# Optimization experiments

Measured on AMD Instinct MI355X. Metric: run time of the kernel, lower is better.

The kernel has to match this reference:

```python
import math
import jax, jax.numpy as jnp
import numpy as np

NUM_HEADS = 8
NUM_LANDMARKS = 64
MP_ITERS = 6


def moore_penrose_iter_pinv(x, iters=MP_ITERS):
    # x: [..., m, m]; iterative Newton-Schulz-style pseudo-inverse
    abs_x = jnp.abs(x)
    col = abs_x.sum(axis=-1)
    row = abs_x.sum(axis=-2)
    z = jnp.swapaxes(x, -1, -2) / (jnp.max(col) * jnp.max(row))
    I = jnp.eye(x.shape[-1], dtype=x.dtype)
    for _ in range(iters):
        xz = x @ z
        z = 0.25 * z @ (13.0 * I - xz @ (15.0 * I - xz @ (7.0 * I - xz)))
    return z


def setup_inputs() -> dict:
    key = jax.random.key(0)
    k_x, k_qkv, k_proj = jax.random.split(key, 3)
    B, T, E = 2, 2048, 512
    x = jax.random.normal(k_x, (B, T, E), dtype=jnp.float32)
    w_qkv = jax.random.normal(k_qkv, (E, 3 * E), dtype=jnp.float32) * 0.02
    b_qkv = jnp.zeros((3 * E,), dtype=jnp.float32)
    w_proj = jax.random.normal(k_proj, (E, E), dtype=jnp.float32) * 0.02
    b_proj = jnp.zeros((E,), dtype=jnp.float32)
    return {"x": x, "w_qkv": w_qkv, "b_qkv": b_qkv, "w_proj": w_proj, "b_proj": b_proj}


def reference(x, w_qkv, b_qkv, w_proj, b_proj):
    B, T, E = x.shape
    H = NUM_HEADS
    M = NUM_LANDMARKS
    hd = E // H
    # T chosen as a multiple of M so the original pad branch is a no-op
    qkv = x @ w_qkv + b_qkv  # [B,T,3E]
    q, k, v = jnp.split(qkv, 3, axis=-1)

    def to_heads(t):
        return t.reshape(B, T, H, hd).transpose(0, 2, 1, 3)  # [B,H,T,hd]

    q = to_heads(q) * (1.0 / math.sqrt(hd))
    k = to_heads(k)
    v = to_heads(v)

    l = T // M  # landmark group size
    q_landmarks = q.reshape(B, H, M, l, hd).mean(axis=3)  # [B,H,M,hd]
    k_landmarks = k.reshape(B, H, M, l, hd).mean(axis=3)  # [B,H,M,hd]

    q_kl = jnp.einsum('bhid,bhjd->bhij', q, k_landmarks)           # [B,H,T,M]
    ql_kl = jnp.einsum('bhid,bhjd->bhij', q_landmarks, k_landmarks)  # [B,H,M,M]
    ql_k = jnp.einsum('bhid,bhjd->bhij', q_landmarks, k)           # [B,H,M,T]

    neg_inf = float('-inf')
    mask_q_kl = jnp.tril(jnp.ones((T, M), dtype=bool))
    mask_ql_kl = jnp.tril(jnp.ones((M, M), dtype=bool))
    mask_ql_k = jnp.tril(jnp.ones((M, T), dtype=bool))

    F_t = jax.nn.softmax(jnp.where(mask_q_kl, q_kl, neg_inf), axis=-1)    # [B,H,T,M]
    A = jax.nn.softmax(jnp.where(mask_ql_kl, ql_kl, neg_inf), axis=-1)    # [B,H,M,M]
    B_t = jax.nn.softmax(jnp.where(mask_ql_k, ql_k, neg_inf), axis=-1)    # [B,H,M,T]

    A_t = moore_penrose_iter_pinv(A, iters=MP_ITERS)

    attn = (F_t @ A_t) @ B_t  # [B,H,T,T] (original materializes this for dropout)
    y = attn @ v              # [B,H,T,hd]
    y = y.transpose(0, 2, 1, 3).reshape(B, T, E)
    return y @ w_proj + b_proj
```

## Files before the change

kernel.cpp:

```cpp
#include <hip/hip_runtime.h>
#include <hip/hip_bf16.h>

#define TB 2048
#define EB 512

using short8 = __attribute__((ext_vector_type(8))) short;
using f32x4  = __attribute__((ext_vector_type(4))) float;

__global__ __launch_bounds__(256) void k_pool(const float* __restrict__ x,
                                              float* __restrict__ xp,
                                              unsigned int* __restrict__ scal_u) {
  if (blockIdx.x == 0 && threadIdx.x == 0) scal_u[0] = 0u;
  int idx = blockIdx.x * 256 + threadIdx.x;
  int b = idx >> 15;
  int rem = idx & 32767;
  int m = rem >> 9;
  int e = rem & 511;
  const float* src = x + (b * TB + m * 32) * EB + e;
  float s = 0.f;
#pragma unroll
  for (int i = 0; i < 32; ++i) s += src[i * EB];
  xp[idx] = s * (1.f / 32.f);
}

__device__ __forceinline__ int swz_idx(int row, int col) {
  return row * 64 + ((((col >> 3) ^ (row & 7)) << 3) | (col & 7));
}

__device__ __forceinline__ void split_bf(float v, ushort& h, ushort& l) {
  __hip_bfloat16 bh = __float2bfloat16(v);
  float fh = __bfloat162float(bh);
  __hip_bfloat16 bl = __float2bfloat16(v - fh);
  h = *(ushort*)&bh;
  l = *(ushort*)&bl;
}

__device__ __forceinline__ void mm_frags(const short8 ah[2], const short8 al[2],
                                         const ushort* bhp, const ushort* blp,
                                         int lane, f32x4 acc[4]) {
  const int g = lane >> 4, li = lane & 15;
#pragma unroll
  for (int nt = 0; nt < 4; ++nt) {
    f32x4 a = acc[nt];
#pragma unroll
    for (int kh = 0; kh < 2; ++kh) {
      int n = nt * 16 + li;
      int k0 = kh * 32 + 8 * g;
      int idx = n * 64 + ((((k0 >> 3) ^ (n & 7)) << 3));
      short8 bh = *(const short8*)&bhp[idx];
      short8 bl = *(const short8*)&blp[idx];
      a = __builtin_amdgcn_mfma_f32_16x16x32_bf16(al[kh], bh, a, 0, 0, 0);
      a = __builtin_amdgcn_mfma_f32_16x16x32_bf16(ah[kh], bl, a, 0, 0, 0);
      a = __builtin_amdgcn_mfma_f32_16x16x32_bf16(ah[kh], bh, a, 0, 0, 0);
    }
    acc[nt] = a;
  }
}

__device__ __forceinline__ void zero_acc(f32x4 acc[4]) {
#pragma unroll
  for (int nt = 0; nt < 4; ++nt) acc[nt] = (f32x4){0.f, 0.f, 0.f, 0.f};
}

__device__ __forceinline__ void softmax_rows(f32x4 s[4], int band, int g, int li,
                                             bool causal, int t0) {
#pragma unroll
  for (int r = 0; r < 4; ++r) {
    int trow = t0 + band + 4 * g + r;
    float m = -1e30f;
    float sv[4];
#pragma unroll
    for (int nt = 0; nt < 4; ++nt) {
      int col = nt * 16 + li;
      bool ok = !causal || (col <= trow);
      sv[nt] = ok ? s[nt][r] : -1e30f;
      m = fmaxf(m, sv[nt]);
    }
    m = fmaxf(m, __shfl_xor(m, 1));
    m = fmaxf(m, __shfl_xor(m, 2));
    m = fmaxf(m, __shfl_xor(m, 4));
    m = fmaxf(m, __shfl_xor(m, 8));
    float su = 0.f;
    float ee[4];
#pragma unroll
    for (int nt = 0; nt < 4; ++nt) {
      ee[nt] = (sv[nt] > -1e29f) ? __expf(sv[nt] - m) : 0.f;
      su += ee[nt];
    }
    su += __shfl_xor(su, 1);
    su += __shfl_xor(su, 2);
    su += __shfl_xor(su, 4);
    su += __shfl_xor(su, 8);
    float inv = 1.f / su;
#pragma unroll
    for (int nt = 0; nt < 4; ++nt) s[nt][r] = ee[nt] * inv;
  }
}

__device__ __forceinline__ void wrP(ushort* hp, ushort* lp, int lane,
                                    const f32x4 acc[4]) {
  const int g = lane >> 4, li = lane & 15;
#pragma unroll
  for (int nt = 0; nt < 4; ++nt) {
    int c = nt * 16 + li;
#pragma unroll
    for (int r = 0; r < 4; ++r) {
      int row = 4 * g + r;
      ushort h, l;
      split_bf(acc[nt][r], h, l);
      int idx = swz_idx(row, c);
      hp[idx] = h;
      lp[idx] = l;
    }
  }
}

__device__ __forceinline__ void ld_pfrags(const ushort* hp, const ushort* lp,
                                          int lane, short8 ah[2], short8 al[2]) {
  const int g = lane >> 4, li = lane & 15;
#pragma unroll
  for (int kh = 0; kh < 2; ++kh) {
    int k0 = kh * 32 + 8 * g;
    int idx = li * 64 + ((((k0 >> 3) ^ (li & 7)) << 3));
    ah[kh] = *(const short8*)&hp[idx];
    al[kh] = *(const short8*)&lp[idx];
  }
}

template <int MODE>
__global__ __launch_bounds__(256) void k_gemm_mfma(const float* __restrict__ A,
                                                   const float* __restrict__ W,
                                                   const float* __restrict__ bias,
                                                   float* __restrict__ o0,
                                                   float* __restrict__ o1) {
  constexpr int LDW = (MODE == 1) ? 512 : 1536;
  __shared__ ushort Ah[4096], Al[4096], Bh[4096], Bl[4096];
  const int tid = threadIdx.x;
  const int lane = tid & 63, w = tid >> 6, band = w * 16;
  int bx, by;
  if constexpr (MODE == 0 || MODE == 1) {
    int bid = blockIdx.x;
    by = ((bid & 7) << 3) | (bid >> 6);
    bx = (bid >> 3) & 7;
  } else {
    bx = blockIdx.x;
    by = blockIdx.y;
  }
  const int n0 = bx * 64, m0 = by * 64;
  const int bcol0 = (MODE == 2 ? 512 : 0) + n0;
  const int g = lane >> 4, li = lane & 15;

  const int arow = tid >> 2, akc = (tid & 3) * 16;
  const int bn = tid & 63, bkc = (tid >> 6) * 16;

  const float* asrc;
  {
    int gr = m0 + arow;
    if constexpr (MODE == 2) {
      asrc = A + ((gr >> 6) * TB + (gr & 63)) * EB;
    } else {
      asrc = A + gr * EB;
    }
  }

  f32x4 acc[4];
  zero_acc(acc);

  for (int k0 = 0; k0 < 512; k0 += 64) {
    if (k0) __syncthreads();
    {
      float av[16];
#pragma unroll
      for (int j = 0; j < 4; ++j)
        *(float4*)&av[j * 4] = *(const float4*)&asrc[k0 + akc + j * 4];
#pragma unroll
      for (int c2 = 0; c2 < 2; ++c2) {
        short8 hv, lv;
#pragma unroll
        for (int i = 0; i < 8; ++i) {
          ushort h, l;
          split_bf(av[c2 * 8 + i], h, l);
          hv[i] = (short)h;
          lv[i] = (short)l;
        }
        int chunk = ((akc >> 3) + c2) ^ (arow & 7);
        int idx = arow * 64 + chunk * 8;
        *(short8*)&Ah[idx] = hv;
        *(short8*)&Al[idx] = lv;
      }
    }
    {
      float bv[16];
#pragma unroll
      for (int i = 0; i < 16; ++i)
        bv[i] = W[(k0 + bkc + i) * LDW + bcol0 + bn];
#pragma unroll
      for (int c2 = 0; c2 < 2; ++c2) {
        short8 hv, lv;
#pragma unroll
        for (int i = 0; i < 8; ++i) {
          ushort h, l;
          split_bf(bv[c2 * 8 + i], h, l);
          hv[i] = (short)h;
          lv[i] = (short)l;
        }
        int chunk = ((bkc >> 3) + c2) ^ (bn & 7);
        int idx = bn * 64 + chunk * 8;
        *(short8*)&Bh[idx] = hv;
        *(short8*)&Bl[idx] = lv;
      }
    }
    __syncthreads();
    short8 a_h[2], a_l[2];
    const int row = band + li;
#pragma unroll
    for (int kh = 0; kh < 2; ++kh) {
      int chunk = ((kh * 32 + 8 * g) >> 3) ^ (row & 7);
      int idx = row * 64 + chunk * 8;
      a_h[kh] = *(const short8*)&Ah[idx];
      a_l[kh] = *(const short8*)&Al[idx];
    }
    mm_frags(a_h, a_l, Bh, Bl, lane, acc);
  }
#pragma unroll
  for (int nt = 0; nt < 4; ++nt) {
#pragma unroll
    for (int r = 0; r < 4; ++r) {
      int trow = band + 4 * g + r;
      int gcol = bcol0 + nt * 16 + li;
      float v = acc[nt][r] + bias[gcol];
      if constexpr (MODE == 0) {
        int rg = m0 + trow;
        int b = rg >> 11, t = rg & 2047;
        int h = gcol >> 6, d = gcol & 63;
        o0[(((b << 3) | h) * 2048 + t) * 64 + d] = v * 0.125f;
      } else if constexpr (MODE == 1) {
        o0[(m0 + trow) * 512 + gcol] = v;
      } else {
        int gr = m0 + trow;
        int b = gr >> 6, t = gr & 63;
        int cloc = gcol - (MODE == 2 ? 512 : 0);
        int which = cloc >> 9;
        int hd_ = cloc & 511;
        int h = hd_ >> 6, d = hd_ & 63;
        int dst = ((b * 8 + h) * 64 + t) * 64 + d;
        if constexpr (MODE == 2) {
          if (which == 0) o0[dst] = v; else o1[dst] = v;
        } else {
          if (which == 0) o0[dst] = v * 0.125f; else o1[dst] = v;
        }
      }
    }
  }
}

__global__ __launch_bounds__(256) void k_a_bv_mfma(
    const float* __restrict__ qlg, const float* __restrict__ klg,
    const float* __restrict__ k64, const float* __restrict__ v64,
    float* __restrict__ A, float* __restrict__ BV,
    unsigned int* __restrict__ scal_u) {
  __shared__ ushort KLh[4096], KLl[4096], Kh[4096], Kl_[4096], VTh[4096], VTl[4096];
  __shared__ ushort Ph[4][1024], Pl[4][1024];
  __shared__ float red[4][64];
  const int bh = blockIdx.x, tid = threadIdx.x;
  const int lane = tid & 63, w = tid >> 6, band = w * 16;
  const int g = lane >> 4, li = lane & 15;
  const int base = bh * 4096;
  {
    int n = tid & 63, kc = (tid >> 6) * 16;
    float a[16], b[16], c[16];
#pragma unroll
    for (int i = 0; i < 16; ++i) {
      a[i] = klg[base + n * 64 + kc + i];
      b[i] = k64[base + n * 64 + kc + i];
      c[i] = v64[base + (kc + i) * 64 + n];
    }
#pragma unroll
    for (int c2 = 0; c2 < 2; ++c2) {
      int idx = n * 64 + ((((kc >> 3) + c2) ^ (n & 7)) << 3);
      short8 hv, lv;
#pragma unroll
      for (int i = 0; i < 8; ++i) { ushort h, l; split_bf(a[c2*8+i], h, l); hv[i]=(short)h; lv[i]=(short)l; }
      *(short8*)&KLh[idx] = hv; *(short8*)&KLl[idx] = lv;
#pragma unroll
      for (int i = 0; i < 8; ++i) { ushort h, l; split_bf(b[c2*8+i], h, l); hv[i]=(short)h; lv[i]=(short)l; }
      *(short8*)&Kh[idx] = hv; *(short8*)&Kl_[idx] = lv;
#pragma unroll
      for (int i = 0; i < 8; ++i) { ushort h, l; split_bf(c[c2*8+i], h, l); hv[i]=(short)h; lv[i]=(short)l; }
      *(short8*)&VTh[idx] = hv; *(short8*)&VTl[idx] = lv;
    }
  }
  short8 q_h[2], q_l[2];
  {
    int row = band + li;
#pragma unroll
    for (int kh = 0; kh < 2; ++kh) {
      int k0 = kh * 32 + 8 * g;
      float tmp[8];
      *(float4*)&tmp[0] = *(const float4*)&qlg[base + row * 64 + k0];
      *(float4*)&tmp[4] = *(const float4*)&qlg[base + row * 64 + k0 + 4];
      short8 hv, lv;
#pragma unroll
      for (int i = 0; i < 8; ++i) { ushort h, l; split_bf(tmp[i], h, l); hv[i]=(short)h; lv[i]=(short)l; }
      q_h[kh] = hv; q_l[kh] = lv;
    }
  }
  __syncthreads();
  f32x4 s1[4];
  zero_acc(s1);
  mm_frags(q_h, q_l, KLh, KLl, lane, s1);
  softmax_rows(s1, band, g, li, true, 0);
#pragma unroll
  for (int nt = 0; nt < 4; ++nt)
#pragma unroll
    for (int r = 0; r < 4; ++r)
      A[base + (band + 4 * g + r) * 64 + nt * 16 + li] = s1[nt][r];
  {
    float part[4];
#pragma unroll
    for (int nt = 0; nt < 4; ++nt) {
      part[nt] = s1[nt][0] + s1[nt][1] + s1[nt][2] + s1[nt][3];
      part[nt] += __shfl_xor(part[nt], 16);
      part[nt] += __shfl_xor(part[nt], 32);
    }
    if (g == 0) {
#pragma unroll
      for (int nt = 0; nt < 4; ++nt) red[w][nt * 16 + li] = part[nt];
    }
    __syncthreads();
    if (tid < 64) {
      float t = red[0][tid] + red[1][tid] + red[2][tid] + red[3][tid];
#pragma unroll
      for (int off = 32; off; off >>= 1) t = fmaxf(t, __shfl_xor(t, off));
      if (tid == 0) atomicMax(scal_u, __float_as_uint(t));
    }
  }
  f32x4 s2[4];
  zero_acc(s2);
  mm_frags(q_h, q_l, Kh, Kl_, lane, s2);
  softmax_rows(s2, band, g, li, true, 0);
  wrP(Ph[w], Pl[w], lane, s2);
  short8 p_h[2], p_l[2];
  ld_pfrags(Ph[w], Pl[w], lane, p_h, p_l);
  f32x4 y[4];
  zero_acc(y);
  mm_frags(p_h, p_l, VTh, VTl, lane, y);
#pragma unroll
  for (int nt = 0; nt < 4; ++nt)
#pragma unroll
    for (int r = 0; r < 4; ++r)
      BV[base + (band + 4 * g + r) * 64 + nt * 16 + li] = y[nt][r];
}

__device__ __forceinline__ void ld_afrags(const ushort* hp, const ushort* lp,
                                          int band, int lane,
                                          short8 ah[2], short8 al[2]) {
  const int g = lane >> 4, li = lane & 15;
  const int row = band + li;
#pragma unroll
  for (int kh = 0; kh < 2; ++kh) {
    int k0 = kh * 32 + 8 * g;
    int idx = row * 64 + ((((k0 >> 3) ^ (row & 7)) << 3));
    ah[kh] = *(const short8*)&hp[idx];
    al[kh] = *(const short8*)&lp[idx];
  }
}

__device__ __forceinline__ void mm_frags0(const short8 ah[2], const short8 al[2],
                                          const ushort* bhp, const ushort* blp,
                                          int lane, f32x4 acc[4]) {
  zero_acc(acc);
  mm_frags(ah, al, bhp, blp, lane, acc);
}

__device__ __forceinline__ void wrT(ushort* hp, ushort* lp, int band, int lane,
                                    const f32x4 acc[4], float cI, float mul) {
  const int g = lane >> 4, li = lane & 15;
  const int r0 = band + 4 * g;
#pragma unroll
  for (int nt = 0; nt < 4; ++nt) {
    int c = nt * 16 + li;
    ushort h[4], l[4];
#pragma unroll
    for (int r = 0; r < 4; ++r) {
      float v = mul * acc[nt][r] + ((r0 + r) == c ? cI : 0.f);
      split_bf(v, h[r], l[r]);
    }
    int idx = c * 64 + (((((r0) >> 3) ^ (c & 7)) << 3) | (r0 & 7));
    *(ushort4*)&hp[idx] = make_ushort4(h[0], h[1], h[2], h[3]);
    *(ushort4*)&lp[idx] = make_ushort4(l[0], l[1], l[2], l[3]);
  }
}

__device__ __forceinline__ void wrN(ushort* hp, ushort* lp, int band, int lane,
                                    const f32x4 acc[4], float mul) {
  const int g = lane >> 4, li = lane & 15;
#pragma unroll
  for (int nt = 0; nt < 4; ++nt) {
    int c = nt * 16 + li;
#pragma unroll
    for (int r = 0; r < 4; ++r) {
      int row = band + 4 * g + r;
      ushort h, l;
      split_bf(mul * acc[nt][r], h, l);
      int idx = swz_idx(row, c);
      hp[idx] = h;
      lp[idx] = l;
    }
  }
}

__global__ __launch_bounds__(256) void k_pinv(const float* __restrict__ A,
                                              const float* __restrict__ BVg,
                                              const unsigned int* __restrict__ scal_u,
                                              float* __restrict__ C) {
  __shared__ ushort ZT_h[4096], ZT_l[4096], ZA_h[4096], ZA_l[4096],
                    PA_h[4096], PA_l[4096], QA_h[4096], QA_l[4096],
                    QB_h[4096], QB_l[4096], BT_h[4096], BT_l[4096];
  const int bh = blockIdx.x, tid = threadIdx.x;
  const int lane = tid & 63, w = tid >> 6, band = w * 16;
  const int base = bh * 4096;
  const float sc = 1.f / __uint_as_float(scal_u[0]);
  const float* Ag = A + base;
  const float* Bg = BVg + base;

  {
    int prow = tid >> 2;
    int pc0 = (tid & 3) * 16;
#pragma unroll 4
    for (int j = 0; j < 16; ++j) {
      int col = pc0 + j;
      float av = Ag[prow * 64 + col] * sc;
      ushort h, l;
      split_bf(av, h, l);
      int i1 = swz_idx(prow, col);
      ZT_h[i1] = h; ZT_l[i1] = l;
      int i2 = swz_idx(col, prow);
      ZA_h[i2] = h; ZA_l[i2] = l;
      float bv = Bg[prow * 64 + col];
      split_bf(bv, h, l);
      BT_h[i2] = h; BT_l[i2] = l;
    }
  }
  short8 a_h[2], a_l[2];
  {
    const int g = lane >> 4, li = lane & 15;
    int row = band + li;
#pragma unroll
    for (int kh = 0; kh < 2; ++kh) {
      int k0 = kh * 32 + 8 * g;
      float tmp[8];
      *(float4*)&tmp[0] = *(const float4*)&Ag[row * 64 + k0];
      *(float4*)&tmp[4] = *(const float4*)&Ag[row * 64 + k0 + 4];
      short8 hv, lv;
#pragma unroll
      for (int i = 0; i < 8; ++i) {
        ushort h, l;
        split_bf(tmp[i], h, l);
        hv[i] = (short)h;
        lv[i] = (short)l;
      }
      a_h[kh] = hv;
      a_l[kh] = lv;
    }
  }
  __syncthreads();

  for (int it = 0; it < 6; ++it) {
    f32x4 acc[4];
    mm_frags0(a_h, a_l, ZT_h, ZT_l, lane, acc);
    wrN(PA_h, PA_l, band, lane, acc, 1.f);
    wrT(QA_h, QA_l, band, lane, acc, 7.f, -1.f);
    __syncthreads();
    short8 p_h[2], p_l[2];
    ld_afrags(PA_h, PA_l, band, lane, p_h, p_l);
    mm_frags0(p_h, p_l, QA_h, QA_l, lane, acc);
    wrT(QB_h, QB_l, band, lane, acc, 15.f, -1.f);
    __syncthreads();
    mm_frags0(p_h, p_l, QB_h, QB_l, lane, acc);
    wrT(QA_h, QA_l, band, lane, acc, 13.f, -1.f);
    __syncthreads();
    short8 z_h[2], z_l[2];
    ld_afrags(ZA_h, ZA_l, band, lane, z_h, z_l);
    mm_frags0(z_h, z_l, QA_h, QA_l, lane, acc);
    wrN(ZA_h, ZA_l, band, lane, acc, 0.25f);
    wrT(ZT_h, ZT_l, band, lane, acc, 0.f, 0.25f);
    __syncthreads();
  }
  {
    short8 z_h[2], z_l[2];
    ld_afrags(ZA_h, ZA_l, band, lane, z_h, z_l);
    f32x4 acc[4];
    mm_frags0(z_h, z_l, BT_h, BT_l, lane, acc);
    const int g = lane >> 4, li = lane & 15;
#pragma unroll
    for (int nt = 0; nt < 4; ++nt) {
#pragma unroll
      for (int r = 0; r < 4; ++r) {
        int row = band + 4 * g + r;
        int col = nt * 16 + li;
        C[base + row * 64 + col] = acc[nt][r];
      }
    }
  }
}

__global__ __launch_bounds__(256) void k_f_y_mfma(const float* __restrict__ q,
                                                  const float* __restrict__ klg,
                                                  const float* __restrict__ C,
                                                  float* __restrict__ yh) {
  __shared__ ushort KLh[4096], KLl[4096], CTh[4096], CTl[4096];
  __shared__ ushort Ph[4][1024], Pl[4][1024];
  const int bh = blockIdx.x;
  const int b = bh >> 3, h = bh & 7;
  const int t0 = blockIdx.y * 64;
  const int tid = threadIdx.x;
  const int lane = tid & 63, w = tid >> 6, band = w * 16;
  const int g = lane >> 4, li = lane & 15;
  const int base = bh * 4096;
  {
    int n = tid & 63, kc = (tid >> 6) * 16;
    float a[16], c[16];
#pragma unroll
    for (int i = 0; i < 16; ++i) {
      a[i] = klg[base + n * 64 + kc + i];
      c[i] = C[base + (kc + i) * 64 + n];
    }
#pragma unroll
    for (int c2 = 0; c2 < 2; ++c2) {
      int idx = n * 64 + ((((kc >> 3) + c2) ^ (n & 7)) << 3);
      short8 hv, lv;
#pragma unroll
      for (int i = 0; i < 8; ++i) { ushort hh, ll; split_bf(a[c2*8+i], hh, ll); hv[i]=(short)hh; lv[i]=(short)ll; }
      *(short8*)&KLh[idx] = hv; *(short8*)&KLl[idx] = lv;
#pragma unroll
      for (int i = 0; i < 8; ++i) { ushort hh, ll; split_bf(c[c2*8+i], hh, ll); hv[i]=(short)hh; lv[i]=(short)ll; }
      *(short8*)&CTh[idx] = hv; *(short8*)&CTl[idx] = lv;
    }
  }
  short8 q_h[2], q_l[2];
  {
    int t = t0 + band + li;
#pragma unroll
    for (int kh = 0; kh < 2; ++kh) {
      int k0 = kh * 32 + 8 * g;
      float tmp[8];
      *(float4*)&tmp[0] = *(const float4*)&q[(bh * 2048 + t) * 64 + k0];
      *(float4*)&tmp[4] = *(const float4*)&q[(bh * 2048 + t) * 64 + k0 + 4];
      short8 hv, lv;
#pragma unroll
      for (int i = 0; i < 8; ++i) { ushort hh, ll; split_bf(tmp[i], hh, ll); hv[i]=(short)hh; lv[i]=(short)ll; }
      q_h[kh] = hv; q_l[kh] = lv;
    }
  }
  __syncthreads();
  f32x4 s[4];
  zero_acc(s);
  mm_frags(q_h, q_l, KLh, KLl, lane, s);
  softmax_rows(s, band, g, li, blockIdx.y == 0, 0);
  wrP(Ph[w], Pl[w], lane, s);
  short8 p_h[2], p_l[2];
  ld_pfrags(Ph[w], Pl[w], lane, p_h, p_l);
  f32x4 y[4];
  zero_acc(y);
  mm_frags(p_h, p_l, CTh, CTl, lane, y);
#pragma unroll
  for (int nt = 0; nt < 4; ++nt)
#pragma unroll
    for (int r = 0; r < 4; ++r) {
      int t = t0 + band + 4 * g + r;
      int d = nt * 16 + li;
      yh[(b * 2048 + t) * 512 + h * 64 + d] = y[nt][r];
    }
}

extern "C" void kernel_launch(void* const* d_in, const int* in_sizes, int n_in,
                              void* d_out, int out_size, void* d_ws, size_t ws_size,
                              hipStream_t stream) {
  const float* x = (const float*)d_in[0];
  const float* w_qkv = (const float*)d_in[1];
  const float* b_qkv = (const float*)d_in[2];
  const float* w_proj = (const float*)d_in[3];
  const float* b_proj = (const float*)d_in[4];
  float* out = (float*)d_out;

  float* ws = (float*)d_ws;
  float* q = ws;
  float* k64 = q + 2097152;
  float* v64 = k64 + 65536;
  float* xp = v64 + 65536;
  float* ql = xp + 65536;
  float* kl = ql + 65536;
  float* Am = kl + 65536;
  float* BV = Am + 65536;
  float* Cm = BV + 65536;
  unsigned int* scal_u = (unsigned int*)(Cm + 65536);
  float* yh = (float*)(scal_u + 64);

  k_pool<<<dim3(256), dim3(256), 0, stream>>>(x, xp, scal_u);
  k_gemm_mfma<0><<<dim3(512), dim3(256), 0, stream>>>(x, w_qkv, b_qkv, q, nullptr);
  k_gemm_mfma<2><<<dim3(16, 2), dim3(256), 0, stream>>>(x, w_qkv, b_qkv, k64, v64);
  k_gemm_mfma<3><<<dim3(16, 2), dim3(256), 0, stream>>>(xp, w_qkv, b_qkv, ql, kl);
  k_a_bv_mfma<<<dim3(16), dim3(256), 0, stream>>>(ql, kl, k64, v64, Am, BV, scal_u);
  k_pinv<<<dim3(16), dim3(256), 0, stream>>>(Am, BV, scal_u, Cm);
  k_f_y_mfma<<<dim3(16, 32), dim3(256), 0, stream>>>(q, kl, Cm, yh);
  k_gemm_mfma<1><<<dim3(512), dim3(256), 0, stream>>>(yh, w_proj, b_proj, out, nullptr);
}
```

Baseline: 159.9 us.

## Merge landmark GEMM launches and prefetch next K-tile into registers

The two small landmark GEMMs (K/V from the first 64 rows and ql/kl from pooled x) are merged into one launch with a doubled grid, where blockIdx.y selects the input, column range and outputs. This drops one kernel launch and lets both small GEMMs run concurrently. The GEMM main loop also now loads the next 64-wide K slice of A and W into registers before the MFMA work, so global load latency overlaps compute. The prefetch adds register pressure, and the variant branching adds some per-thread index arithmetic.

```diff
diff --git a/kernel.cpp b/kernel.cpp
--- a/kernel.cpp
+++ b/kernel.cpp
@@ -129,10 +129,13 @@
 
 template <int MODE>
 __global__ __launch_bounds__(256) void k_gemm_mfma(const float* __restrict__ A,
+                                                   const float* __restrict__ A2,
                                                    const float* __restrict__ W,
                                                    const float* __restrict__ bias,
                                                    float* __restrict__ o0,
-                                                   float* __restrict__ o1) {
+                                                   float* __restrict__ o1,
+                                                   float* __restrict__ o2,
+                                                   float* __restrict__ o3) {
   constexpr int LDW = (MODE == 1) ? 512 : 1536;
   __shared__ ushort Ah[4096], Al[4096], Bh[4096], Bl[4096];
   const int tid = threadIdx.x;
@@ -146,8 +149,10 @@
     bx = blockIdx.x;
     by = blockIdx.y;
   }
-  const int n0 = bx * 64, m0 = by * 64;
-  const int bcol0 = (MODE == 2 ? 512 : 0) + n0;
+  const int variant = (MODE == 2) ? (by >> 1) : 0;
+  const int m0 = (MODE == 2) ? ((by & 1) * 64) : by * 64;
+  const int bcol0 = (MODE == 2) ? (variant == 0 ? 512 + bx * 64 : bx * 64)
+                                : bx * 64;
   const int g = lane >> 4, li = lane & 15;
 
   const int arow = tid >> 2, akc = (tid & 3) * 16;
@@ -157,7 +162,8 @@
   {
     int gr = m0 + arow;
     if constexpr (MODE == 2) {
-      asrc = A + ((gr >> 6) * TB + (gr & 63)) * EB;
+      asrc = (variant == 0) ? (A + ((gr >> 6) * TB + (gr & 63)) * EB)
+                            : (A2 + gr * EB);
     } else {
       asrc = A + gr * EB;
     }
@@ -166,51 +172,55 @@
   f32x4 acc[4];
   zero_acc(acc);
 
+  float av[16], bv[16];
+#pragma unroll
+  for (int j = 0; j < 4; ++j)
+    *(float4*)&av[j * 4] = *(const float4*)&asrc[akc + j * 4];
+#pragma unroll
+  for (int i = 0; i < 16; ++i) bv[i] = W[(bkc + i) * LDW + bcol0 + bn];
+
+#pragma unroll
   for (int k0 = 0; k0 < 512; k0 += 64) {
     if (k0) __syncthreads();
-    {
-      float av[16];
+#pragma unroll
+    for (int c2 = 0; c2 < 2; ++c2) {
+      short8 hv, lv;
+#pragma unroll
+      for (int i = 0; i < 8; ++i) {
+        ushort h, l;
+        split_bf(av[c2 * 8 + i], h, l);
+        hv[i] = (short)h;
+        lv[i] = (short)l;
+      }
+      int chunk = ((akc >> 3) + c2) ^ (arow & 7);
+      int idx = arow * 64 + chunk * 8;
+      *(short8*)&Ah[idx] = hv;
+      *(short8*)&Al[idx] = lv;
+    }
+#pragma unroll
+    for (int c2 = 0; c2 < 2; ++c2) {
+      short8 hv, lv;
+#pragma unroll
+      for (int i = 0; i < 8; ++i) {
+        ushort h, l;
+        split_bf(bv[c2 * 8 + i], h, l);
+        hv[i] = (short)h;
+        lv[i] = (short)l;
+      }
+      int chunk = ((bkc >> 3) + c2) ^ (bn & 7);
+      int idx = bn * 64 + chunk * 8;
+      *(short8*)&Bh[idx] = hv;
+      *(short8*)&Bl[idx] = lv;
+    }
+    __syncthreads();
+    if (k0 + 64 < 512) {
 #pragma unroll
       for (int j = 0; j < 4; ++j)
-        *(float4*)&av[j * 4] = *(const float4*)&asrc[k0 + akc + j * 4];
-#pragma unroll
-      for (int c2 = 0; c2 < 2; ++c2) {
-        short8 hv, lv;
-#pragma unroll
-        for (int i = 0; i < 8; ++i) {
-          ushort h, l;
-          split_bf(av[c2 * 8 + i], h, l);
-          hv[i] = (short)h;
-          lv[i] = (short)l;
-        }
-        int chunk = ((akc >> 3) + c2) ^ (arow & 7);
-        int idx = arow * 64 + chunk * 8;
-        *(short8*)&Ah[idx] = hv;
-        *(short8*)&Al[idx] = lv;
-      }
-    }
-    {
-      float bv[16];
+        *(float4*)&av[j * 4] = *(const float4*)&asrc[k0 + 64 + akc + j * 4];
 #pragma unroll
       for (int i = 0; i < 16; ++i)
-        bv[i] = W[(k0 + bkc + i) * LDW + bcol0 + bn];
-#pragma unroll
-      for (int c2 = 0; c2 < 2; ++c2) {
-        short8 hv, lv;
-#pragma unroll
-        for (int i = 0; i < 8; ++i) {
-          ushort h, l;
-          split_bf(bv[c2 * 8 + i], h, l);
-          hv[i] = (short)h;
-          lv[i] = (short)l;
-        }
-        int chunk = ((bkc >> 3) + c2) ^ (bn & 7);
-        int idx = bn * 64 + chunk * 8;
-        *(short8*)&Bh[idx] = hv;
-        *(short8*)&Bl[idx] = lv;
-      }
-    }
-    __syncthreads();
+        bv[i] = W[(k0 + 64 + bkc + i) * LDW + bcol0 + bn];
+    }
     short8 a_h[2], a_l[2];
     const int row = band + li;
 #pragma unroll
@@ -239,15 +249,15 @@
       } else {
         int gr = m0 + trow;
         int b = gr >> 6, t = gr & 63;
-        int cloc = gcol - (MODE == 2 ? 512 : 0);
+        int cloc = (variant == 0) ? (gcol - 512) : gcol;
         int which = cloc >> 9;
         int hd_ = cloc & 511;
         int h = hd_ >> 6, d = hd_ & 63;
         int dst = ((b * 8 + h) * 64 + t) * 64 + d;
-        if constexpr (MODE == 2) {
+        if (variant == 0) {
           if (which == 0) o0[dst] = v; else o1[dst] = v;
         } else {
-          if (which == 0) o0[dst] = v * 0.125f; else o1[dst] = v;
+          if (which == 0) o2[dst] = v * 0.125f; else o3[dst] = v;
         }
       }
     }
@@ -598,11 +608,13 @@
   float* yh = (float*)(scal_u + 64);
 
   k_pool<<<dim3(256), dim3(256), 0, stream>>>(x, xp, scal_u);
-  k_gemm_mfma<0><<<dim3(512), dim3(256), 0, stream>>>(x, w_qkv, b_qkv, q, nullptr);
-  k_gemm_mfma<2><<<dim3(16, 2), dim3(256), 0, stream>>>(x, w_qkv, b_qkv, k64, v64);
-  k_gemm_mfma<3><<<dim3(16, 2), dim3(256), 0, stream>>>(xp, w_qkv, b_qkv, ql, kl);
+  k_gemm_mfma<0><<<dim3(512), dim3(256), 0, stream>>>(x, nullptr, w_qkv, b_qkv,
+                                                      q, nullptr, nullptr, nullptr);
+  k_gemm_mfma<2><<<dim3(16, 4), dim3(256), 0, stream>>>(x, xp, w_qkv, b_qkv,
+                                                        k64, v64, ql, kl);
   k_a_bv_mfma<<<dim3(16), dim3(256), 0, stream>>>(ql, kl, k64, v64, Am, BV, scal_u);
   k_pinv<<<dim3(16), dim3(256), 0, stream>>>(Am, BV, scal_u, Cm);
   k_f_y_mfma<<<dim3(16, 32), dim3(256), 0, stream>>>(q, kl, Cm, yh);
-  k_gemm_mfma<1><<<dim3(512), dim3(256), 0, stream>>>(yh, w_proj, b_proj, out, nullptr);
-}
+  k_gemm_mfma<1><<<dim3(512), dim3(256), 0, stream>>>(yh, nullptr, w_proj, b_proj,
+                                                      out, nullptr, nullptr, nullptr);
+}
```

Result: faster. 143.8 us (-10.1%).
